# Optimization experiments

Measured on AMD Instinct MI355X. Metric: run time of the kernel, lower is better.

Reference implementation:

```python
import jax, jax.numpy as jnp
import numpy as np

# Model dims (see shape_source)
N, S, E, NMP, H, O = 20000, 16, 160000, 2, 4, 64
D_FEAT, E_DIM, PREP, NCLS, B = 64, 32, 128, 8, 4096
D1 = H * O  # 256, node/edge dim after layer 0


def setup_inputs() -> dict:
    key = jax.random.key(0)
    ks = jax.random.split(key, 24)
    g = lambda i, shape, fan: jax.random.normal(ks[i], shape, jnp.float32) * (fan ** -0.5)
    return {
        "feats": jax.random.normal(ks[0], (N, D_FEAT), jnp.float32),
        "edge_emb": jax.random.normal(ks[1], (NMP, E, E_DIM), jnp.float32),
        "W_prep0": g(2, (D_FEAT, PREP), D_FEAT),
        "W_prep1": g(3, (D_FEAT, PREP), D_FEAT),
        "edge_prep_w": g(4, (NMP, E_DIM, PREP), E_DIM),
        "edge_wq_l0": g(5, (NMP, H, PREP, O), PREP),
        "edge_wk_l0": g(6, (NMP, H, PREP, O), PREP),
        "edge_wq_l1": g(7, (NMP, H, D1, O), D1),
        "edge_wk_l1": g(8, (NMP, H, D1, O), D1),
        "node_wq_l0": g(9, (NMP, H, PREP, O), PREP),
        "node_wk_l0": g(10, (NMP, H, PREP, O), PREP),
        "node_wq_l1": g(11, (NMP, H, D1, O), D1),
        "node_wk_l1": g(12, (NMP, H, D1, O), D1),
        "Wg": g(13, (2 * D1, PREP), 2 * D1),
        "vg": g(14, (PREP,), PREP),
        "W_fc": g(15, (2 * D1, NCLS), 2 * D1),
        "b_fc": jnp.zeros((NCLS,), jnp.float32),
        "node2edge_idx": jax.random.randint(ks[20], (NMP, N, S), 0, E),
        "edge_node_adj": jax.random.randint(ks[21], (NMP, E, 2), 0, N),
        "train_ids": jax.random.randint(ks[22], (B,), 0, N),
    }


def _attn_agg(x_q, x_neigh, wq, wk):
    """Multi-head attention aggregator.
    x_q [M,d], x_neigh [M,s,d2], wq [H,d,O], wk [H,d2,O] -> [M, H*O]."""
    q = jnp.einsum('md,hdo->mho', x_q, wq)
    k = jnp.einsum('msd,hdo->msho', x_neigh, wk)
    logits = jnp.einsum('mho,msho->mhs', q, k) / np.float32(np.sqrt(O))
    a = jax.nn.softmax(logits, axis=-1)
    agg = jnp.einsum('mhs,msho->mho', a, k)
    out = jax.nn.elu(q + agg)
    return out.reshape(out.shape[0], H * O)


def reference(feats, edge_emb, W_prep0, W_prep1, edge_prep_w,
              edge_wq_l0, edge_wk_l0, edge_wq_l1, edge_wk_l1,
              node_wq_l0, node_wk_l0, node_wq_l1, node_wk_l1,
              Wg, vg, W_fc, b_fc,
              node2edge_idx, edge_node_adj, train_ids):
    e_wq, e_wk = [edge_wq_l0, edge_wq_l1], [edge_wk_l0, edge_wk_l1]
    n_wq, n_wk = [node_wq_l0, node_wq_l1], [node_wk_l0, node_wk_l1]
    outs = []
    for mp in range(NMP):  # small fixed count of message-passing branches
        dummy = feats @ W_prep0          # prep layer 0  [N,PREP]
        all_feats = feats @ W_prep1      # prep layer 1  [N,PREP]
        all_edges = edge_emb[mp] @ edge_prep_w[mp]  # [E,PREP]
        skip = []
        for l in range(2):  # depth
            # edge update: gather endpoint node feats [E,2,d], attend, concat heads
            neigh_nodes = all_feats[edge_node_adj[mp]]
            next_edges = _attn_agg(all_edges, neigh_nodes, e_wq[l][mp], e_wk[l][mp])
            # node update: gather incident edge feats [N,S,d] from OLD all_edges
            src = dummy if l == 0 else all_feats
            neigh_edges = all_edges[node2edge_idx[mp]]
            next_feats = _attn_agg(src, neigh_edges, n_wq[l][mp], n_wk[l][mp])
            skip.append(next_feats)
            all_feats, all_edges = next_feats, next_edges
        outs.append(jnp.concatenate(skip, axis=-1)[train_ids])  # [B, 2*D1]
    x = jnp.stack(outs, 0)  # [NMP, B, 512]
    # gated metapath aggregation (mp_agg): softmax over mp axis
    gate = jax.nn.softmax(jnp.einsum('mbe,e->mb', jnp.tanh(jnp.einsum('mbd,de->mbe', x, Wg)), vg), axis=0)
    pooled = jnp.einsum('mb,mbd->bd', gate, x)
    logits = pooled @ W_fc + b_fc  # [B, NCLS]
    return logits, gate
```

## Files before the change

### kernel.cpp

```cpp
#include <hip/hip_runtime.h>
#include <hip/hip_bf16.h>
#include <math.h>

#define N_NODES 20000
#define S_NE    16
#define E_EDGES 160000
#define NMP     2
#define H_HEADS 4
#define O_DIM   64
#define D_FEAT  64
#define E_DIMC  32
#define PREP    128
#define NCLS    8
#define B_TR    4096
#define D1      256
#define NSLOT   (B_TR * S_NE)

#define LDA0    132
#define LDA1    260
#define NPAD    264

typedef __hip_bfloat16 bf16;
typedef unsigned short u16;
typedef __attribute__((ext_vector_type(8))) short s8v;
// ... 115 lines not shown
        if (combo == 0) { qeh[dst] = hh; qel[dst] = ll; }
        else            { k0h[dst] = hh; k0l[dst] = ll; }
    } else if (combo == 2) {
        wkn[(size_t)mp * 64 * D1 + (size_t)r * D1 + n] = acc;
    } else {
        wq0[(size_t)mp * 64 * D1 + (size_t)r * D1 + n] = acc;
    }
}
__global__ void k_precomb2(const void* epw, const void* ewq, const void* nwk0,
                           const void* Wp1, const void* ewk,
                           const void* Wp0, const void* nwq0,
                           float* wkn, float* wq0,
                           u16* qeh, u16* qel, u16* k0h, u16* k0l,
                           const int* flag) {
    if (*flag == 1) precomb2_body<float>(epw, ewq, nwk0, Wp1, ewk, Wp0, nwq0, wkn, wq0, qeh, qel, k0h, k0l);
    else            precomb2_body<bf16 >(epw, ewq, nwk0, Wp1, ewk, Wp0, nwq0, wkn, wq0, qeh, qel, k0h, k0l);
}

template <typename T>
__device__ void embsplit_body(const void* emb, u16* eh, u16* el) {
    size_t idx = (size_t)blockIdx.x * 256 + threadIdx.x;
    if (idx >= (size_t)NMP * E_EDGES * E_DIMC) return;
    float v = ldv<T>(emb, idx);
    u16 hh, ll; splitbf(v, hh, ll);
    eh[idx] = hh; el[idx] = ll;
}
__global__ void k_embsplit(const void* emb, u16* eh, u16* el, const int* flag) {
    if (*flag == 1) embsplit_body<float>(emb, eh, el);
    else            embsplit_body<bf16 >(emb, eh, el);
}

template <typename T>
__device__ void wt1_body(const void* wk1, const void* wq1,
                         u16* kth, u16* ktl, u16* qth, u16* qtl) {
    int idx = blockIdx.x * 256 + threadIdx.x;
    int k = idx & 255, n = (idx >> 8) & 255;
    int wsel = (idx >> 16) & 1, mp = idx >> 17;
    size_t src = (size_t)mp * (H_HEADS * D1 * O_DIM) + (size_t)(n >> 6) * (D1 * O_DIM)
               + (size_t)k * O_DIM + (n & 63);
    float v = ldv<T>(wsel ? wq1 : wk1, src);
    u16 h, l; splitbf(v, h, l);
    size_t dst = (size_t)mp * 65536 + (size_t)n * 256 + k;
    if (wsel) { qth[dst] = h; qtl[dst] = l; }
    else      { kth[dst] = h; ktl[dst] = l; }
}
__global__ void k_wt1(const void* wk1, const void* wq1,
                      u16* kth, u16* ktl, u16* qth, u16* qtl, const int* flag) {
    if (*flag == 1) wt1_body<float>(wk1, wq1, kth, ktl, qth, qtl);
    else            wt1_body<bf16 >(wk1, wq1, kth, ktl, qth, qtl);
}

template <typename T>
__device__ void wgt_body(const void* Wg, u16* gh, u16* gl) {
    int idx = blockIdx.x * 256 + threadIdx.x;
    int n = idx >> 9, k = idx & 511;
    float v = ldv<T>(Wg, (size_t)k * PREP + n);
    u16 h, l; splitbf(v, h, l);
    gh[(size_t)n * 512 + k] = h;
    gl[(size_t)n * 512 + k] = l;
}
__global__ void k_wgt(const void* Wg, u16* gh, u16* gl, const int* flag) {
    if (*flag == 1) wgt_body<float>(Wg, gh, gl);
    else            wgt_body<bf16 >(Wg, gh, gl);
}

template <typename TA, typename TB>
__device__ void gemm_body(const void* A, size_t aOff, const int* Aidx, int strideA,
                          const void* B, int sH, int sD,
                          float* C, int ldC, int M, int K) {
    int bm = blockIdx.x * 64;
    int h  = blockIdx.y;
    int t  = threadIdx.x;
    int tx = t & 15, ty = t >> 4;

    __shared__ float As[32][68];
    __shared__ float Bs[32][68];

    float acc[4][4] = {{0.f}};
    int arow = t >> 3, kq = (t & 7) * 4;
    int brow = t >> 4, nq = (t & 15) * 4;

    for (int k0 = 0; k0 < K; k0 += 32) {
        #pragma unroll
        for (int c = 0; c < 2; ++c) {
            int rm = arow + 32 * c;
            int gr = bm + rm;
            gr = (gr < M) ? gr : 0;
            size_t row = Aidx ? (size_t)Aidx[gr] : (size_t)gr;
            float4 a = ld4<TA>(A, aOff + row * strideA + k0 + kq);
            As[kq + 0][rm] = a.x; As[kq + 1][rm] = a.y;
            As[kq + 2][rm] = a.z; As[kq + 3][rm] = a.w;
        }
        #pragma unroll
        for (int c = 0; c < 2; ++c) {
            int rk = brow + 16 * c;
            float4 b = ld4<TB>(B, (size_t)h * sH + (size_t)(k0 + rk) * sD + nq);
            *(float4*)&Bs[rk][nq] = b;
        }
        __syncthreads();
        #pragma unroll
        for (int kk = 0; kk < 32; ++kk) {
            float4 av = *(const float4*)&As[kk][ty * 4];
            float4 bv = *(const float4*)&Bs[kk][tx * 4];
            float am[4] = {av.x, av.y, av.z, av.w};
            #pragma unroll
            for (int i = 0; i < 4; ++i) {
                acc[i][0] += am[i] * bv.x; acc[i][1] += am[i] * bv.y;
                acc[i][2] += am[i] * bv.z; acc[i][3] += am[i] * bv.w;
            }
        }
        __syncthreads();
    }
    #pragma unroll
    for (int i = 0; i < 4; ++i) {
        int m = bm + ty * 4 + i;
        if (m < M) {
            float4 st; st.x = acc[i][0]; st.y = acc[i][1];
            st.z = acc[i][2]; st.w = acc[i][3];
            *(float4*)&C[(size_t)m * ldC + h * 64 + tx * 4] = st;
        }
    }
}
__global__ __launch_bounds__(256) void k_gemm_rf(
        const void* A, size_t aOff, const int* Aidx, int strideA,
        const float* B, int sH, int sD, float* C, int ldC, int M, int K,
        const int* flag) {
    if (*flag == 1) gemm_body<float, float>(A, aOff, Aidx, strideA, B, sH, sD, C, ldC, M, K);
    else            gemm_body<bf16,  float>(A, aOff, Aidx, strideA, B, sH, sD, C, ldC, M, K);
}

template <int K, bool G>
__device__ __forceinline__ void mfma_core(
        const u16* __restrict__ Ah, const u16* __restrict__ Al,
        const int* __restrict__ rows,
        const u16* __restrict__ Bh, const u16* __restrict__ Bl,
        int rbase, int bn, int lane, f4v acc[4][4]) {
    int fr = lane & 15;
    int kq = (lane >> 4) * 8;
    #pragma unroll
    for (int i = 0; i < 4; ++i)
        #pragma unroll
        for (int j = 0; j < 4; ++j) acc[i][j] = f4v{0.f, 0.f, 0.f, 0.f};
    #pragma unroll 2
    for (int k0 = 0; k0 < K; k0 += 32) {
        s8v ah[4], al[4], bh[4], bl[4];
        #pragma unroll
        for (int i = 0; i < 4; ++i) {
            size_t arow;
            if constexpr (G) arow = (size_t)rows[rbase + i * 16 + fr];
            else             arow = (size_t)(rbase + i * 16 + fr);
            size_t ao = arow * K + k0 + kq;
            ah[i] = *(const s8v*)(Ah + ao);
            al[i] = *(const s8v*)(Al + ao);
            size_t bo = (size_t)(bn + i * 16 + fr) * K + k0 + kq;
            bh[i] = *(const s8v*)(Bh + bo);
            bl[i] = *(const s8v*)(Bl + bo);
        }
        #pragma unroll
        for (int i = 0; i < 4; ++i)
            #pragma unroll
            for (int j = 0; j < 4; ++j) {
                acc[i][j] = __builtin_amdgcn_mfma_f32_16x16x32_bf16(al[i], bh[j], acc[i][j], 0, 0, 0);
                acc[i][j] = __builtin_amdgcn_mfma_f32_16x16x32_bf16(ah[i], bl[j], acc[i][j], 0, 0, 0);
                acc[i][j] = __builtin_amdgcn_mfma_f32_16x16x32_bf16(ah[i], bh[j], acc[i][j], 0, 0, 0);
            }
    }
}

template <int K>
__global__ __launch_bounds__(256) void k_mfma(
        const u16* __restrict__ Ah, const u16* __restrict__ Al,
        const u16* __restrict__ Bh, const u16* __restrict__ Bl,
        float* __restrict__ C, int ldC) {
    int w = threadIdx.x >> 6, lane = threadIdx.x & 63;
    int bm = blockIdx.x * 128 + (w & 1) * 64;
    int bn = blockIdx.y * 128 + (w >> 1) * 64;
    f4v acc[4][4];
    mfma_core<K, false>(Ah, Al, nullptr, Bh, Bl, bm, bn, lane, acc);
    int cn = lane & 15, cr = (lane >> 4) * 4;
    #pragma unroll
    for (int i = 0; i < 4; ++i) {
        int m0 = bm + i * 16 + cr;
        #pragma unroll
        for (int j = 0; j < 4; ++j) {
            int n = bn + j * 16 + cn;
            #pragma unroll
            for (int r = 0; r < 4; ++r)
                C[(size_t)(m0 + r) * ldC + n] = acc[i][j][r];
        }
    }
}

template <int K, bool G>
__global__ __launch_bounds__(256) void k_mfma_nattn(
        const u16* __restrict__ Ah, const u16* __restrict__ Al,
        const int* __restrict__ rows,
        const u16* __restrict__ Bh, const u16* __restrict__ Bl,
        const float* __restrict__ q,
        u16* __restrict__ o0h, u16* __restrict__ o0l,
        float* __restrict__ xrow, int xoff,
        u16* __restrict__ xh, u16* __restrict__ xl) {
    int w = threadIdx.x >> 6, lane = threadIdx.x & 63;
    int rbase = blockIdx.x * 128 + (w & 1) * 64;
    int bn = blockIdx.y * 128 + (w >> 1) * 64;
    f4v acc[4][4];
    mfma_core<K, G>(Ah, Al, rows, Bh, Bl, rbase, bn, lane, acc);

    int cn = lane & 15, grp = lane >> 4;
    #pragma unroll
    for (int i = 0; i < 4; ++i) {
        int b = (rbase >> 4) + i;
        float qv[4];
        #pragma unroll
        for (int j = 0; j < 4; ++j)
            qv[j] = q[(size_t)b * D1 + bn + j * 16 + cn];
        float lg[4];
        #pragma unroll
        for (int r = 0; r < 4; ++r) {
            float p = 0.f;
            #pragma unroll
            for (int j = 0; j < 4; ++j) p += acc[i][j][r] * qv[j];
            lg[r] = grp16_sum(p) * 0.125f;
        }
        float mx = fmaxf(fmaxf(lg[0], lg[1]), fmaxf(lg[2], lg[3]));
        mx = fmaxf(mx, __shfl_xor(mx, 16, 64));
        mx = fmaxf(mx, __shfl_xor(mx, 32, 64));
        float e[4], s = 0.f;
        #pragma unroll
        for (int r = 0; r < 4; ++r) { e[r] = expf(lg[r] - mx); s += e[r]; }
        s += __shfl_xor(s, 16, 64);
        s += __shfl_xor(s, 32, 64);
        float inv = 1.f / s;
        #pragma unroll
        for (int j = 0; j < 4; ++j) {
            float ag = e[0] * acc[i][j][0] + e[1] * acc[i][j][1]
                     + e[2] * acc[i][j][2] + e[3] * acc[i][j][3];
            ag += __shfl_xor(ag, 16, 64);
            ag += __shfl_xor(ag, 32, 64);
            float v = eluf(qv[j] + ag * inv);
            if (grp == 0) {
                int col = bn + j * 16 + cn;
                xrow[(size_t)b * (2 * D1) + xoff + col] = v;
                u16 hh, ll; splitbf(v, hh, ll);
                xh[(size_t)b * (2 * D1) + xoff + col] = hh;
                xl[(size_t)b * (2 * D1) + xoff + col] = ll;
                if (o0h) {
                    o0h[(size_t)b * D1 + col] = hh;
                    o0l[(size_t)b * D1 + col] = ll;
                }
            }
        }
    }
}

__global__ __launch_bounds__(512, 4) void k_mega(
        const u16* __restrict__ Ah, const u16* __restrict__ Al,
        const int* __restrict__ rows,
        const u16* __restrict__ qBh, const u16* __restrict__ qBl,
        const float* __restrict__ Kn,
        const int* __restrict__ adjA, const int* __restrict__ adjB,
        const u16* __restrict__ kBh, const u16* __restrict__ kBl,
        const float* __restrict__ q,
        float* __restrict__ xrow,
        u16* __restrict__ xh, u16* __restrict__ xl) {
    __shared__ u16 sh_[64][NPAD];
    __shared__ u16 sl_[64][NPAD];
    int w = threadIdx.x >> 6, lane = threadIdx.x & 63;
    int wr = w & 1, wc = w >> 1;
    int blk = blockIdx.x * 64;
    int rbase = blk + wr * 32;
    int bn = wc * 64;
    int fr = lane & 15, kq = (lane >> 4) * 8;
    int cn = lane & 15, cr = (lane >> 4) * 4;

    int raA[2][4], raB[2][4];
    #pragma unroll
    for (int i = 0; i < 2; ++i)
        #pragma unroll
        for (int r = 0; r < 4; ++r) {
            int slot = rbase + i * 16 + cr + r;
            raA[i][r] = adjA[slot] * D1;
            raB[i][r] = adjB[slot] * D1;
        }

    f4v acc[2][4];
    #pragma unroll
    for (int i = 0; i < 2; ++i)
        #pragma unroll
        for (int j = 0; j < 4; ++j) acc[i][j] = f4v{0.f, 0.f, 0.f, 0.f};
    {
        s8v ah[2], al[2], bh[4], bl[4];
        #pragma unroll
        for (int i = 0; i < 2; ++i) {
            size_t ao = (size_t)rows[rbase + i * 16 + fr] * E_DIMC + kq;
            ah[i] = *(const s8v*)(Ah + ao);
            al[i] = *(const s8v*)(Al + ao);
        }
        #pragma unroll
        for (int j = 0; j < 4; ++j) {
            size_t bo = (size_t)(bn + j * 16 + fr) * E_DIMC + kq;
            bh[j] = *(const s8v*)(qBh + bo);
            bl[j] = *(const s8v*)(qBl + bo);
        }
        #pragma unroll
        for (int i = 0; i < 2; ++i)
            #pragma unroll
            for (int j = 0; j < 4; ++j) {
                acc[i][j] = __builtin_amdgcn_mfma_f32_16x16x32_bf16(al[i], bh[j], acc[i][j], 0, 0, 0);
                acc[i][j] = __builtin_amdgcn_mfma_f32_16x16x32_bf16(ah[i], bl[j], acc[i][j], 0, 0, 0);
                acc[i][j] = __builtin_amdgcn_mfma_f32_16x16x32_bf16(ah[i], bh[j], acc[i][j], 0, 0, 0);
            }
    }

    #pragma unroll
    for (int i = 0; i < 2; ++i) {
        #pragma unroll
        for (int r = 0; r < 4; ++r) {
            int lrow = wr * 32 + i * 16 + cr + r;
            size_t ra = (size_t)raA[i][r];
            size_t rb = (size_t)raB[i][r];
            float kA[4], kB[4];
            float pA = 0.f, pB = 0.f;
            #pragma unroll
            for (int j = 0; j < 4; ++j) {
                int col = bn + j * 16 + cn;
                kA[j] = Kn[ra + col];
                kB[j] = Kn[rb + col];
                pA += acc[i][j][r] * kA[j];
                pB += acc[i][j][r] * kB[j];
            }
            float lA = grp16_sum(pA) * 0.125f;
            float lB = grp16_sum(pB) * 0.125f;
            float m = fmaxf(lA, lB);
            float eA = expf(lA - m), eB = expf(lB - m);
            float inv = 1.f / (eA + eB);
            #pragma unroll
            for (int j = 0; j < 4; ++j) {
                int col = bn + j * 16 + cn;
                float v = eluf(acc[i][j][r] + (eA * kA[j] + eB * kB[j]) * inv);
                u16 hh, ll; splitbf(v, hh, ll);
                sh_[lrow][col] = hh;
                sl_[lrow][col] = ll;
            }
        }
    }
    __syncthreads();

    #pragma unroll
    for (int i = 0; i < 2; ++i)
        #pragma unroll
        for (int j = 0; j < 4; ++j) acc[i][j] = f4v{0.f, 0.f, 0.f, 0.f};
    #pragma unroll 2
    for (int k0 = 0; k0 < 256; k0 += 32) {
        s8v ah[2], al[2], bh[4], bl[4];
        #pragma unroll
        for (int i = 0; i < 2; ++i) {
            int lr = wr * 32 + i * 16 + fr;
            ah[i] = *(const s8v*)&sh_[lr][k0 + kq];
            al[i] = *(const s8v*)&sl_[lr][k0 + kq];
        }
        #pragma unroll
        for (int j = 0; j < 4; ++j) {
            size_t bo = (size_t)(bn + j * 16 + fr) * 256 + k0 + kq;
            bh[j] = *(const s8v*)(kBh + bo);
            bl[j] = *(const s8v*)(kBl + bo);
        }
        #pragma unroll
        for (int i = 0; i < 2; ++i)
            #pragma unroll
            for (int j = 0; j < 4; ++j) {
                acc[i][j] = __builtin_amdgcn_mfma_f32_16x16x32_bf16(al[i], bh[j], acc[i][j], 0, 0, 0);
                acc[i][j] = __builtin_amdgcn_mfma_f32_16x16x32_bf16(ah[i], bl[j], acc[i][j], 0, 0, 0);
                acc[i][j] = __builtin_amdgcn_mfma_f32_16x16x32_bf16(ah[i], bh[j], acc[i][j], 0, 0, 0);
            }
    }

    int grp = lane >> 4;
    #pragma unroll
    for (int i = 0; i < 2; ++i) {
        int b = (rbase >> 4) + i;
        float qv[4];
        #pragma unroll
        for (int j = 0; j < 4; ++j)
            qv[j] = q[(size_t)b * D1 + bn + j * 16 + cn];
        float lg[4];
        #pragma unroll
        for (int r = 0; r < 4; ++r) {
            float p = 0.f;
            #pragma unroll
            for (int j = 0; j < 4; ++j) p += acc[i][j][r] * qv[j];
            lg[r] = grp16_sum(p) * 0.125f;
        }
        float mx = fmaxf(fmaxf(lg[0], lg[1]), fmaxf(lg[2], lg[3]));
        mx = fmaxf(mx, __shfl_xor(mx, 16, 64));
        mx = fmaxf(mx, __shfl_xor(mx, 32, 64));
        float e[4], s = 0.f;
        #pragma unroll
        for (int r = 0; r < 4; ++r) { e[r] = expf(lg[r] - mx); s += e[r]; }
        s += __shfl_xor(s, 16, 64);
        s += __shfl_xor(s, 32, 64);
        float inv = 1.f / s;
        #pragma unroll
        for (int j = 0; j < 4; ++j) {
            float ag = e[0] * acc[i][j][0] + e[1] * acc[i][j][1]
                     + e[2] * acc[i][j][2] + e[3] * acc[i][j][3];
            ag += __shfl_xor(ag, 16, 64);
            ag += __shfl_xor(ag, 32, 64);
            float v = eluf(qv[j] + ag * inv);
            if (grp == 0) {
                int col = bn + j * 16 + cn;
                xrow[(size_t)b * (2 * D1) + D1 + col] = v;
                u16 hh, ll; splitbf(v, hh, ll);
                xh[(size_t)b * (2 * D1) + D1 + col] = hh;
                xl[(size_t)b * (2 * D1) + D1 + col] = ll;
            }
        }
    }
}

__global__ void k_slot_setup(const int* __restrict__ n2e_mp,
                             const int* __restrict__ adj_mp,
                             const int* __restrict__ tid,
                             int* __restrict__ eid,
                             int* __restrict__ adjA,
                             int* __restrict__ adjB) {
    int i = blockIdx.x * blockDim.x + threadIdx.x;
    if (i >= NSLOT) return;
    int b = i >> 4, s = i & 15;
    int e = n2e_mp[(size_t)tid[b] * S_NE + s];
    eid[i] = e;
    adjA[i] = adj_mp[(size_t)e * 2 + 0];
    adjB[i] = adj_mp[(size_t)e * 2 + 1];
}

template <typename T>
__device__ void gate_fin_body(const float* gmat, const void* vg, float* gate_pre) {
    int row = blockIdx.x;
    int t = threadIdx.x;
    float v = tanhf(gmat[(size_t)row * PREP + t]) * ldv<T>(vg, t);
    __shared__ float red[128];
    red[t] = v;
    __syncthreads();
    for (int s = 64; s > 0; s >>= 1) { if (t < s) red[t] += red[t + s]; __syncthreads(); }
    if (t == 0) gate_pre[row] = red[0];
}
__global__ void k_gate_fin(const float* gmat, const void* vg, float* gate_pre,
                           const int* flag) {
    if (*flag == 1) gate_fin_body<float>(gmat, vg, gate_pre);
    else            gate_fin_body<bf16 >(gmat, vg, gate_pre);
}

template <typename T>
__device__ void gate_dir_body(const float* xcat, const void* Wg, const void* vg,
                              float* gate_pre) {
    int mb = blockIdx.x;
    int t = threadIdx.x;
    __shared__ float xr[2 * D1];
    for (int idx = t; idx < 2 * D1; idx += 128) xr[idx] = xcat[(size_t)mb * (2 * D1) + idx];
    __syncthreads();
    float acc = 0.f;
    for (int d = 0; d < 2 * D1; ++d) acc += xr[d] * ldv<T>(Wg, (size_t)d * PREP + t);
    float gp = tanhf(acc) * ldv<T>(vg, t);
    __shared__ float red[128];
    red[t] = gp;
    __syncthreads();
// ... 295 lines not shown
    const void* e_wk0       = d_in[6];
    const void* n_wq0       = d_in[9];
    const void* n_wk0       = d_in[10];
    const void* n_wq1       = d_in[11];
    const void* n_wk1       = d_in[12];
    const void* Wg          = d_in[13];
    const void* vg          = d_in[14];
    const void* Wfc         = d_in[15];
    const void* bfc         = d_in[16];
    const int*  n2e         = (const int*)d_in[17];
    const int*  adj         = (const int*)d_in[18];
    const int*  tid         = (const int*)d_in[19];

    float* ws   = (float*)d_ws;
    int*   flag = (int*)ws;
    float* base = ws + 4;
    size_t avail = (ws_size >= 16) ? (ws_size - 16) / 4 : 0;

    k_detect<<<1, 64, 0, stream>>>((const unsigned*)feats, flag);

    size_t off = 0;
    auto alloc = [&](size_t n) { size_t o = off; off += (n + 3) & ~(size_t)3; return o; };
    size_t o_xcat = alloc((size_t)NMP * B_TR * 2 * D1);
    size_t o_gmat = alloc((size_t)NMP * B_TR * PREP);
    size_t o_gpre = alloc(NMP * B_TR);
    size_t o_wkn  = alloc(NMP * 64 * D1);
    size_t o_wq0  = alloc(NMP * 64 * D1);
    size_t o_qeh  = alloc(NMP * 256 * 32 / 2);
    size_t o_qel  = alloc(NMP * 256 * 32 / 2);
    size_t o_k0h  = alloc(NMP * 256 * 32 / 2);
    size_t o_k0l  = alloc(NMP * 256 * 32 / 2);
    size_t o_ebh  = alloc((size_t)NMP * E_EDGES * E_DIMC / 2);
    size_t o_ebl  = alloc((size_t)NMP * E_EDGES * E_DIMC / 2);
    size_t o_Kn   = alloc((size_t)N_NODES * D1);
    size_t o_q0   = alloc((size_t)B_TR * D1);
    size_t o_Q1   = alloc((size_t)B_TR * D1);
    size_t o_eid  = alloc(NSLOT);
    size_t o_adjA = alloc(NSLOT);
    size_t o_adjB = alloc(NSLOT);
    size_t o_o0h  = alloc((size_t)B_TR * D1 / 2);
    size_t o_o0l  = alloc((size_t)B_TR * D1 / 2);
    size_t o_xh   = alloc((size_t)NMP * B_TR * D1);
    size_t o_xl   = alloc((size_t)NMP * B_TR * D1);
    size_t o_wk1h = alloc((size_t)NMP * 32768);
    size_t o_wk1l = alloc((size_t)NMP * 32768);
    size_t o_wq1h = alloc((size_t)NMP * 32768);
    size_t o_wq1l = alloc((size_t)NMP * 32768);
    size_t o_wgh  = alloc(32768);
    size_t o_wgl  = alloc(32768);
    size_t fixed = off;

    int CH = (fixed <= avail) ? B_TR : 0;

    if (CH > 0) {
        float* xcat = base + o_xcat;
        float* gmat = base + o_gmat;
        float* gpre = base + o_gpre;
        float* wkn  = base + o_wkn;
        float* wq0  = base + o_wq0;
        u16*   qeh  = (u16*)(base + o_qeh);
        u16*   qel  = (u16*)(base + o_qel);
        u16*   k0h  = (u16*)(base + o_k0h);
        u16*   k0l  = (u16*)(base + o_k0l);
        u16*   ebh  = (u16*)(base + o_ebh);
        u16*   ebl  = (u16*)(base + o_ebl);
        float* Kn   = base + o_Kn;
        float* q0   = base + o_q0;
        float* Q1   = base + o_Q1;
        int*   eid  = (int*)(base + o_eid);
        int*   adjA = (int*)(base + o_adjA);
        int*   adjB = (int*)(base + o_adjB);
        u16*   o0h  = (u16*)(base + o_o0h);
        u16*   o0l  = (u16*)(base + o_o0l);
        u16*   xh   = (u16*)(base + o_xh);
        u16*   xl   = (u16*)(base + o_xl);
        u16*   wk1h = (u16*)(base + o_wk1h);
        u16*   wk1l = (u16*)(base + o_wk1l);
        u16*   wq1h = (u16*)(base + o_wq1h);
        u16*   wq1l = (u16*)(base + o_wq1l);
        u16*   wgh  = (u16*)(base + o_wgh);
        u16*   wgl  = (u16*)(base + o_wgl);
        int NC = B_TR / CH;

        k_precomb2<<<384, 256, 0, stream>>>(edge_prep_w, e_wq0, n_wk0, W_prep1,
                                            e_wk0, W_prep0, n_wq0,
                                            wkn, wq0, qeh, qel, k0h, k0l, flag);
        k_embsplit<<<(NMP * E_EDGES * E_DIMC + 255) / 256, 256, 0, stream>>>(
            edge_emb, ebh, ebl, flag);
        k_wt1<<<1024, 256, 0, stream>>>(n_wk1, n_wq1, wk1h, wk1l, wq1h, wq1l, flag);
        k_wgt<<<256, 256, 0, stream>>>(Wg, wgh, wgl, flag);

        for (int mp = 0; mp < NMP; ++mp) {
            k_slot_setup<<<(NSLOT + 255) / 256, 256, 0, stream>>>(
                n2e + (size_t)mp * N_NODES * S_NE,
                adj + (size_t)mp * E_EDGES * 2,
                tid, eid, adjA, adjB);

            k_gemm_rf<<<dim3((N_NODES + 63) / 64, 4), 256, 0, stream>>>(
                feats, 0, nullptr, D_FEAT, wkn + (size_t)mp * 64 * D1,
                64, D1, Kn, D1, N_NODES, D_FEAT, flag);
            k_gemm_rf<<<dim3(B_TR / 64, 4), 256, 0, stream>>>(
                feats, 0, tid, D_FEAT, wq0 + (size_t)mp * 64 * D1,
                64, D1, q0, D1, B_TR, D_FEAT, flag);

            const u16* ebh_mp = ebh + (size_t)mp * E_EDGES * E_DIMC;
            const u16* ebl_mp = ebl + (size_t)mp * E_EDGES * E_DIMC;

            for (int c = 0; c < NC; ++c) {
                int c0 = c * CH;
                int MS = CH * S_NE;
                k_mfma_nattn<32, true><<<dim3(MS / 128, 2), 256, 0, stream>>>(
                    ebh_mp, ebl_mp, eid + (size_t)c0 * S_NE,
                    k0h + (size_t)mp * 8192, k0l + (size_t)mp * 8192,
                    q0 + (size_t)c0 * D1, o0h, o0l,
                    xcat + ((size_t)mp * B_TR + c0) * 2 * D1, 0,
                    xh + ((size_t)mp * B_TR + c0) * 2 * D1,
                    xl + ((size_t)mp * B_TR + c0) * 2 * D1);
                k_mfma<256><<<dim3(CH / 128, 2), 256, 0, stream>>>(
                    o0h, o0l, wq1h + (size_t)mp * 65536, wq1l + (size_t)mp * 65536,
                    Q1, D1);
                k_mega<<<MS / 64, 512, 0, stream>>>(
                    ebh_mp, ebl_mp, eid + (size_t)c0 * S_NE,
                    qeh + (size_t)mp * 8192, qel + (size_t)mp * 8192,
                    Kn, adjA + (size_t)c0 * S_NE, adjB + (size_t)c0 * S_NE,
                    wk1h + (size_t)mp * 65536, wk1l + (size_t)mp * 65536,
                    Q1,
                    xcat + ((size_t)mp * B_TR + c0) * 2 * D1,
                    xh + ((size_t)mp * B_TR + c0) * 2 * D1,
                    xl + ((size_t)mp * B_TR + c0) * 2 * D1);
            }
        }
        k_mfma<512><<<dim3(NMP * B_TR / 128, 1), 256, 0, stream>>>(
            xh, xl, wgh, wgl, gmat, PREP);
        k_gate_fin<<<NMP * B_TR, 128, 0, stream>>>(gmat, vg, gpre, flag);
        k_final<<<B_TR, 64, 0, stream>>>(xcat, gpre, Wfc, bfc, d_out, flag);
    } else {
        size_t f_off = 0;
        auto falloc = [&](size_t n) { size_t o = f_off; f_off += (n + 3) & ~(size_t)3; return o; };
        float* af0  = base + falloc((size_t)N_NODES * PREP);
        float* xcat = base + falloc((size_t)NMP * B_TR * 2 * D1);
        float* gpre = base + falloc(NMP * B_TR);

        k_prep_nodes<float><<<(N_NODES * 32 + 255) / 256, 256, 0, stream>>>(
            feats, W_prep1, af0, flag);
        k_prep_nodes<bf16><<<(N_NODES * 32 + 255) / 256, 256, 0, stream>>>(
            feats, W_prep1, af0, flag);

        for (int mp = 0; mp < NMP; ++mp) {
            #define FUSED_ARGS(esz)                                                   \
                feats,                                                                \
                (const char*)edge_emb + (esz) * (size_t)mp * E_EDGES * E_DIMC,        \
                W_prep0,                                                              \
                (const char*)edge_prep_w + (esz) * (size_t)mp * E_DIMC * PREP,        \
                (const char*)e_wq0 + (esz) * (size_t)mp * H_HEADS * PREP * O_DIM,     \
                (const char*)e_wk0 + (esz) * (size_t)mp * H_HEADS * PREP * O_DIM,     \
                (const char*)n_wq0 + (esz) * (size_t)mp * H_HEADS * PREP * O_DIM,     \
                (const char*)n_wk0 + (esz) * (size_t)mp * H_HEADS * PREP * O_DIM,     \
                (const char*)n_wq1 + (esz) * (size_t)mp * H_HEADS * D1 * O_DIM,       \
                (const char*)n_wk1 + (esz) * (size_t)mp * H_HEADS * D1 * O_DIM,       \
                n2e + (size_t)mp * N_NODES * S_NE,                                    \
                adj + (size_t)mp * E_EDGES * 2,                                       \
                tid, af0, xcat + (size_t)mp * B_TR * 2 * D1, flag
            k_fused<float><<<B_TR, 256, 0, stream>>>(FUSED_ARGS(4));
            k_fused<bf16><<<B_TR, 256, 0, stream>>>(FUSED_ARGS(2));
// ... 7 lines not shown
```

Baseline: 528.9 us.

## Fuse layer-0 node attention and Q1 projection into mega kernel

Merges the layer-0 node attention kernel, the Q1 GEMM and the layer-1 mega kernel into one kernel per metapath. The layer-0 output now stays in shared memory, and Q1 is computed in-block by an fp32 dot product against a transposed fp32 copy of wq1. This removes the chunk loop, two launches per chunk and the intermediate global buffers. In exchange, the Q1 projection moves from split-bf16 MFMA to scalar FMAs, with each block re-reading the full 256x256 weight column set, and shared memory use grows.

Result: no change. 532.7 us (+0.7%).

```diff
diff --git a/kernel.cpp b/kernel.cpp
--- a/kernel.cpp
+++ b/kernel.cpp
@@ -171,7 +171,7 @@
 
 template <typename T>
 __device__ void wt1_body(const void* wk1, const void* wq1,
-                         u16* kth, u16* ktl, u16* qth, u16* qtl) {
+                         u16* kth, u16* ktl, u16* qth, u16* qtl, float* wq1f) {
     int idx = blockIdx.x * 256 + threadIdx.x;
     int k = idx & 255, n = (idx >> 8) & 255;
     int wsel = (idx >> 16) & 1, mp = idx >> 17;
@@ -180,13 +180,18 @@
     float v = ldv<T>(wsel ? wq1 : wk1, src);
     u16 h, l; splitbf(v, h, l);
     size_t dst = (size_t)mp * 65536 + (size_t)n * 256 + k;
-    if (wsel) { qth[dst] = h; qtl[dst] = l; }
-    else      { kth[dst] = h; ktl[dst] = l; }
+    if (wsel) {
+        qth[dst] = h; qtl[dst] = l;
+        wq1f[(size_t)mp * 65536 + (size_t)k * 256 + n] = v;
+    } else {
+        kth[dst] = h; ktl[dst] = l;
+    }
 }
 __global__ void k_wt1(const void* wk1, const void* wq1,
-                      u16* kth, u16* ktl, u16* qth, u16* qtl, const int* flag) {
-    if (*flag == 1) wt1_body<float>(wk1, wq1, kth, ktl, qth, qtl);
-    else            wt1_body<bf16 >(wk1, wq1, kth, ktl, qth, qtl);
+                      u16* kth, u16* ktl, u16* qth, u16* qtl, float* wq1f,
+                      const int* flag) {
+    if (*flag == 1) wt1_body<float>(wk1, wq1, kth, ktl, qth, qtl, wq1f);
+    else            wt1_body<bf16 >(wk1, wq1, kth, ktl, qth, qtl, wq1f);
 }
 
 template <typename T>
@@ -330,29 +335,81 @@
     }
 }
 
-template <int K, bool G>
-__global__ __launch_bounds__(256) void k_mfma_nattn(
+__global__ __launch_bounds__(512, 4) void k_mega2(
         const u16* __restrict__ Ah, const u16* __restrict__ Al,
         const int* __restrict__ rows,
-        const u16* __restrict__ Bh, const u16* __restrict__ Bl,
-        const float* __restrict__ q,
-        u16* __restrict__ o0h, u16* __restrict__ o0l,
-        float* __restrict__ xrow, int xoff,
+        const u16* __restrict__ k0Bh, const u16* __restrict__ k0Bl,
+        const u16* __restrict__ qBh,  const u16* __restrict__ qBl,
+        const float* __restrict__ q0,
+        const float* __restrict__ Kn,
+        const int* __restrict__ adjA, const int* __restrict__ adjB,
+        const u16* __restrict__ kBh, const u16* __restrict__ kBl,
+        const float* __restrict__ wq1f,
+        float* __restrict__ xrow,
         u16* __restrict__ xh, u16* __restrict__ xl) {
+    __shared__ u16 sh_[64][NPAD];
+    __shared__ u16 sl_[64][NPAD];
+    __shared__ float s_o0[4][D1];
+    __shared__ float s_q1[4][D1];
     int w = threadIdx.x >> 6, lane = threadIdx.x & 63;
-    int rbase = blockIdx.x * 128 + (w & 1) * 64;
-    int bn = blockIdx.y * 128 + (w >> 1) * 64;
-    f4v acc[4][4];
-    mfma_core<K, G>(Ah, Al, rows, Bh, Bl, rbase, bn, lane, acc);
-
-    int cn = lane & 15, grp = lane >> 4;
-    #pragma unroll
-    for (int i = 0; i < 4; ++i) {
-        int b = (rbase >> 4) + i;
+    int wr = w & 1, wc = w >> 1;
+    int blk = blockIdx.x * 64;
+    int rbase = blk + wr * 32;
+    int bn = wc * 64;
+    int fr = lane & 15, kq = (lane >> 4) * 8;
+    int cn = lane & 15, cr = (lane >> 4) * 4;
+    int grp = lane >> 4;
+
+    int raA[2][4], raB[2][4];
+    #pragma unroll
+    for (int i = 0; i < 2; ++i)
+        #pragma unroll
+        for (int r = 0; r < 4; ++r) {
+            int slot = rbase + i * 16 + cr + r;
+            raA[i][r] = adjA[slot] * D1;
+            raB[i][r] = adjB[slot] * D1;
+        }
+
+    s8v ebh2[2], ebl2[2];
+    #pragma unroll
+    for (int i = 0; i < 2; ++i) {
+        size_t ao = (size_t)rows[rbase + i * 16 + fr] * E_DIMC + kq;
+        ebh2[i] = *(const s8v*)(Ah + ao);
+        ebl2[i] = *(const s8v*)(Al + ao);
+    }
+
+    f4v acc[2][4];
+
+    #pragma unroll
+    for (int i = 0; i < 2; ++i)
+        #pragma unroll
+        for (int j = 0; j < 4; ++j) acc[i][j] = f4v{0.f, 0.f, 0.f, 0.f};
+    {
+        s8v bh[4], bl[4];
+        #pragma unroll
+        for (int j = 0; j < 4; ++j) {
+            size_t bo = (size_t)(bn + j * 16 + fr) * E_DIMC + kq;
+            bh[j] = *(const s8v*)(k0Bh + bo);
+            bl[j] = *(const s8v*)(k0Bl + bo);
+        }
+        #pragma unroll
+        for (int i = 0; i < 2; ++i)
+            #pragma unroll
+            for (int j = 0; j < 4; ++j) {
+                acc[i][j] = __builtin_amdgcn_mfma_f32_16x16x32_bf16(ebl2[i], bh[j], acc[i][j], 0, 0, 0);
+                acc[i][j] = __builtin_amdgcn_mfma_f32_16x16x32_bf16(ebh2[i], bl[j], acc[i][j], 0, 0, 0);
+                acc[i][j] = __builtin_amdgcn_mfma_f32_16x16x32_bf16(ebh2[i], bh[j], acc[i][j], 0, 0, 0);
+            }
+    }
+
+    #pragma unroll
+    for (int i = 0; i < 2; ++i) {
+        int b  = (rbase >> 4) + i;
+        int lb = wr * 2 + i;
         float qv[4];
         #pragma unroll
         for (int j = 0; j < 4; ++j)
-            qv[j] = q[(size_t)b * D1 + bn + j * 16 + cn];
+            qv[j] = q0[(size_t)b * D1 + bn + j * 16 + cn];
         float lg[4];
         #pragma unroll
         for (int r = 0; r < 4; ++r) {
@@ -379,62 +436,22 @@
             float v = eluf(qv[j] + ag * inv);
             if (grp == 0) {
                 int col = bn + j * 16 + cn;
-                xrow[(size_t)b * (2 * D1) + xoff + col] = v;
+                xrow[(size_t)b * (2 * D1) + col] = v;
                 u16 hh, ll; splitbf(v, hh, ll);
-                xh[(size_t)b * (2 * D1) + xoff + col] = hh;
-                xl[(size_t)b * (2 * D1) + xoff + col] = ll;
-                if (o0h) {
-                    o0h[(size_t)b * D1 + col] = hh;
-                    o0l[(size_t)b * D1 + col] = ll;
-                }
-            }
-        }
-    }
-}
-
-__global__ __launch_bounds__(512, 4) void k_mega(
-        const u16* __restrict__ Ah, const u16* __restrict__ Al,
-        const int* __restrict__ rows,
-        const u16* __restrict__ qBh, const u16* __restrict__ qBl,
-        const float* __restrict__ Kn,
-        const int* __restrict__ adjA, const int* __restrict__ adjB,
-        const u16* __restrict__ kBh, const u16* __restrict__ kBl,
-        const float* __restrict__ q,
-        float* __restrict__ xrow,
-        u16* __restrict__ xh, u16* __restrict__ xl) {
-    __shared__ u16 sh_[64][NPAD];
-    __shared__ u16 sl_[64][NPAD];
-    int w = threadIdx.x >> 6, lane = threadIdx.x & 63;
-    int wr = w & 1, wc = w >> 1;
-    int blk = blockIdx.x * 64;
-    int rbase = blk + wr * 32;
-    int bn = wc * 64;
-    int fr = lane & 15, kq = (lane >> 4) * 8;
-    int cn = lane & 15, cr = (lane >> 4) * 4;
-
-    int raA[2][4], raB[2][4];
-    #pragma unroll
-    for (int i = 0; i < 2; ++i)
-        #pragma unroll
-        for (int r = 0; r < 4; ++r) {
-            int slot = rbase + i * 16 + cr + r;
-            raA[i][r] = adjA[slot] * D1;
-            raB[i][r] = adjB[slot] * D1;
-        }
-
-    f4v acc[2][4];
+                xh[(size_t)b * (2 * D1) + col] = hh;
+                xl[(size_t)b * (2 * D1) + col] = ll;
+                s_o0[lb][col] = v;
+            }
+        }
+    }
+    __syncthreads();
+
     #pragma unroll
     for (int i = 0; i < 2; ++i)
         #pragma unroll
         for (int j = 0; j < 4; ++j) acc[i][j] = f4v{0.f, 0.f, 0.f, 0.f};
     {
-        s8v ah[2], al[2], bh[4], bl[4];
-        #pragma unroll
-        for (int i = 0; i < 2; ++i) {
-            size_t ao = (size_t)rows[rbase + i * 16 + fr] * E_DIMC + kq;
-            ah[i] = *(const s8v*)(Ah + ao);
-            al[i] = *(const s8v*)(Al + ao);
-        }
+        s8v bh[4], bl[4];
         #pragma unroll
         for (int j = 0; j < 4; ++j) {
             size_t bo = (size_t)(bn + j * 16 + fr) * E_DIMC + kq;
@@ -445,10 +462,24 @@
         for (int i = 0; i < 2; ++i)
             #pragma unroll
             for (int j = 0; j < 4; ++j) {
-                acc[i][j] = __builtin_amdgcn_mfma_f32_16x16x32_bf16(al[i], bh[j], acc[i][j], 0, 0, 0);
-                acc[i][j] = __builtin_amdgcn_mfma_f32_16x16x32_bf16(ah[i], bl[j], acc[i][j], 0, 0, 0);
-                acc[i][j] = __builtin_amdgcn_mfma_f32_16x16x32_bf16(ah[i], bh[j], acc[i][j], 0, 0, 0);
-            }
+                acc[i][j] = __builtin_amdgcn_mfma_f32_16x16x32_bf16(ebl2[i], bh[j], acc[i][j], 0, 0, 0);
+                acc[i][j] = __builtin_amdgcn_mfma_f32_16x16x32_bf16(ebh2[i], bl[j], acc[i][j], 0, 0, 0);
+                acc[i][j] = __builtin_amdgcn_mfma_f32_16x16x32_bf16(ebh2[i], bh[j], acc[i][j], 0, 0, 0);
+            }
+    }
+
+    {
+        int lb0 = wr * 2, lb1 = lb0 + 1;
+        float q1a = 0.f, q1b = 0.f;
+        const float* wcol = wq1f + bn + lane;
+        #pragma unroll 4
+        for (int k = 0; k < D1; ++k) {
+            float wv = wcol[(size_t)k * D1];
+            q1a += s_o0[lb0][k] * wv;
+            q1b += s_o0[lb1][k] * wv;
+        }
+        s_q1[lb0][bn + lane] = q1a;
+        s_q1[lb1][bn + lane] = q1b;
     }
 
     #pragma unroll
@@ -514,14 +545,14 @@
             }
     }
 
-    int grp = lane >> 4;
     #pragma unroll
     for (int i = 0; i < 2; ++i) {
-        int b = (rbase >> 4) + i;
+        int b  = (rbase >> 4) + i;
+        int lb = wr * 2 + i;
         float qv[4];
         #pragma unroll
         for (int j = 0; j < 4; ++j)
-            qv[j] = q[(size_t)b * D1 + bn + j * 16 + cn];
+            qv[j] = s_q1[lb][bn + j * 16 + cn];
         float lg[4];
         #pragma unroll
         for (int r = 0; r < 4; ++r) {
@@ -933,18 +964,16 @@
     size_t o_ebl  = alloc((size_t)NMP * E_EDGES * E_DIMC / 2);
     size_t o_Kn   = alloc((size_t)N_NODES * D1);
     size_t o_q0   = alloc((size_t)B_TR * D1);
-    size_t o_Q1   = alloc((size_t)B_TR * D1);
     size_t o_eid  = alloc(NSLOT);
     size_t o_adjA = alloc(NSLOT);
     size_t o_adjB = alloc(NSLOT);
-    size_t o_o0h  = alloc((size_t)B_TR * D1 / 2);
-    size_t o_o0l  = alloc((size_t)B_TR * D1 / 2);
     size_t o_xh   = alloc((size_t)NMP * B_TR * D1);
     size_t o_xl   = alloc((size_t)NMP * B_TR * D1);
     size_t o_wk1h = alloc((size_t)NMP * 32768);
     size_t o_wk1l = alloc((size_t)NMP * 32768);
     size_t o_wq1h = alloc((size_t)NMP * 32768);
     size_t o_wq1l = alloc((size_t)NMP * 32768);
+    size_t o_wq1f = alloc((size_t)NMP * 65536);
     size_t o_wgh  = alloc(32768);
     size_t o_wgl  = alloc(32768);
     size_t fixed = off;
@@ -965,28 +994,26 @@
         u16*   ebl  = (u16*)(base + o_ebl);
         float* Kn   = base + o_Kn;
         float* q0   = base + o_q0;
-        float* Q1   = base + o_Q1;
         int*   eid  = (int*)(base + o_eid);
         int*   adjA = (int*)(base + o_adjA);
         int*   adjB = (int*)(base + o_adjB);
-        u16*   o0h  = (u16*)(base + o_o0h);
-        u16*   o0l  = (u16*)(base + o_o0l);
         u16*   xh   = (u16*)(base + o_xh);
         u16*   xl   = (u16*)(base + o_xl);
         u16*   wk1h = (u16*)(base + o_wk1h);
         u16*   wk1l = (u16*)(base + o_wk1l);
         u16*   wq1h = (u16*)(base + o_wq1h);
         u16*   wq1l = (u16*)(base + o_wq1l);
+        float* wq1f = base + o_wq1f;
         u16*   wgh  = (u16*)(base + o_wgh);
         u16*   wgl  = (u16*)(base + o_wgl);
-        int NC = B_TR / CH;
 
         k_precomb2<<<384, 256, 0, stream>>>(edge_prep_w, e_wq0, n_wk0, W_prep1,
                                             e_wk0, W_prep0, n_wq0,
                                             wkn, wq0, qeh, qel, k0h, k0l, flag);
         k_embsplit<<<(NMP * E_EDGES * E_DIMC + 255) / 256, 256, 0, stream>>>(
             edge_emb, ebh, ebl, flag);
-        k_wt1<<<1024, 256, 0, stream>>>(n_wk1, n_wq1, wk1h, wk1l, wq1h, wq1l, flag);
+        k_wt1<<<1024, 256, 0, stream>>>(n_wk1, n_wq1, wk1h, wk1l, wq1h, wq1l,
+                                        wq1f, flag);
         k_wgt<<<256, 256, 0, stream>>>(Wg, wgh, wgl, flag);
 
         for (int mp = 0; mp < NMP; ++mp) {
@@ -1002,32 +1029,18 @@
                 feats, 0, tid, D_FEAT, wq0 + (size_t)mp * 64 * D1,
                 64, D1, q0, D1, B_TR, D_FEAT, flag);
 
-            const u16* ebh_mp = ebh + (size_t)mp * E_EDGES * E_DIMC;
-            const u16* ebl_mp = ebl + (size_t)mp * E_EDGES * E_DIMC;
-
-            for (int c = 0; c < NC; ++c) {
-                int c0 = c * CH;
-                int MS = CH * S_NE;
-                k_mfma_nattn<32, true><<<dim3(MS / 128, 2), 256, 0, stream>>>(
-                    ebh_mp, ebl_mp, eid + (size_t)c0 * S_NE,
-                    k0h + (size_t)mp * 8192, k0l + (size_t)mp * 8192,
-                    q0 + (size_t)c0 * D1, o0h, o0l,
-                    xcat + ((size_t)mp * B_TR + c0) * 2 * D1, 0,
-                    xh + ((size_t)mp * B_TR + c0) * 2 * D1,
-                    xl + ((size_t)mp * B_TR + c0) * 2 * D1);
-                k_mfma<256><<<dim3(CH / 128, 2), 256, 0, stream>>>(
-                    o0h, o0l, wq1h + (size_t)mp * 65536, wq1l + (size_t)mp * 65536,
-                    Q1, D1);
-                k_mega<<<MS / 64, 512, 0, stream>>>(
-                    ebh_mp, ebl_mp, eid + (size_t)c0 * S_NE,
-                    qeh + (size_t)mp * 8192, qel + (size_t)mp * 8192,
-                    Kn, adjA + (size_t)c0 * S_NE, adjB + (size_t)c0 * S_NE,
-                    wk1h + (size_t)mp * 65536, wk1l + (size_t)mp * 65536,
-                    Q1,
-                    xcat + ((size_t)mp * B_TR + c0) * 2 * D1,
-                    xh + ((size_t)mp * B_TR + c0) * 2 * D1,
-                    xl + ((size_t)mp * B_TR + c0) * 2 * D1);
-            }
+            k_mega2<<<NSLOT / 64, 512, 0, stream>>>(
+                ebh + (size_t)mp * E_EDGES * E_DIMC,
+                ebl + (size_t)mp * E_EDGES * E_DIMC,
+                eid,
+                k0h + (size_t)mp * 8192, k0l + (size_t)mp * 8192,
+                qeh + (size_t)mp * 8192, qel + (size_t)mp * 8192,
+                q0, Kn, adjA, adjB,
+                wk1h + (size_t)mp * 65536, wk1l + (size_t)mp * 65536,
+                wq1f + (size_t)mp * 65536,
+                xcat + (size_t)mp * B_TR * 2 * D1,
+                xh + (size_t)mp * B_TR * 2 * D1,
+                xl + (size_t)mp * B_TR * 2 * D1);
         }
         k_mfma<512><<<dim3(NMP * B_TR / 128, 1), 256, 0, stream>>>(
             xh, xl, wgh, wgl, gmat, PREP);
```

## Batch both metapaths and all chunks into single grid-z launches

Applied to the files above, without the earlier changes.

Replaces the host loop over metapaths and batch chunks with single launches that use blockIdx.z to select the metapath, and processes the whole batch at once. Intermediate buffers (Kn, q0, Q1, slot indices, o0) are enlarged to hold both metapaths. This cuts kernel launch count and gives each kernel a larger grid for better GPU occupancy, at the cost of more scratch memory and a larger working set.

Result: faster. 492.5 us, median of 3 (-6.9%).

```diff
diff --git a/kernel.cpp b/kernel.cpp
--- a/kernel.cpp
+++ b/kernel.cpp
@@ -205,7 +205,7 @@
 
 template <typename TA, typename TB>
 __device__ void gemm_body(const void* A, size_t aOff, const int* Aidx, int strideA,
-                          const void* B, int sH, int sD,
+                          const float* B, int sH, int sD,
                           float* C, int ldC, int M, int K) {
     int bm = blockIdx.x * 64;
     int h  = blockIdx.y;
@@ -233,7 +233,7 @@
         #pragma unroll
         for (int c = 0; c < 2; ++c) {
             int rk = brow + 16 * c;
-            float4 b = ld4<TB>(B, (size_t)h * sH + (size_t)(k0 + rk) * sD + nq);
+            float4 b = ld4<float>(B, (size_t)h * sH + (size_t)(k0 + rk) * sD + nq);
             *(float4*)&Bs[rk][nq] = b;
         }
         __syncthreads();
@@ -262,10 +262,13 @@
 }
 __global__ __launch_bounds__(256) void k_gemm_rf(
         const void* A, size_t aOff, const int* Aidx, int strideA,
-        const float* B, int sH, int sD, float* C, int ldC, int M, int K,
+        const float* B, size_t bStride, int sH, int sD,
+        float* C, size_t cStride, int ldC, int M, int K,
         const int* flag) {
-    if (*flag == 1) gemm_body<float, float>(A, aOff, Aidx, strideA, B, sH, sD, C, ldC, M, K);
-    else            gemm_body<bf16,  float>(A, aOff, Aidx, strideA, B, sH, sD, C, ldC, M, K);
+    const float* Bz = B + (size_t)blockIdx.z * bStride;
+    float* Cz = C + (size_t)blockIdx.z * cStride;
+    if (*flag == 1) gemm_body<float, float>(A, aOff, Aidx, strideA, Bz, sH, sD, Cz, ldC, M, K);
+    else            gemm_body<bf16,  float>(A, aOff, Aidx, strideA, Bz, sH, sD, Cz, ldC, M, K);
 }
 
 template <int K, bool G>
@@ -330,20 +333,60 @@
     }
 }
 
-template <int K, bool G>
-__global__ __launch_bounds__(256) void k_mfma_nattn(
-        const u16* __restrict__ Ah, const u16* __restrict__ Al,
-        const int* __restrict__ rows,
-        const u16* __restrict__ Bh, const u16* __restrict__ Bl,
-        const float* __restrict__ q,
-        u16* __restrict__ o0h, u16* __restrict__ o0l,
-        float* __restrict__ xrow, int xoff,
-        u16* __restrict__ xh, u16* __restrict__ xl) {
+__global__ __launch_bounds__(256) void k_q1(
+        const u16* __restrict__ o0h, const u16* __restrict__ o0l,
+        const u16* __restrict__ qth, const u16* __restrict__ qtl,
+        float* __restrict__ Q1) {
+    int mp = blockIdx.z;
+    const u16* Ah = o0h + (size_t)mp * B_TR * D1;
+    const u16* Al = o0l + (size_t)mp * B_TR * D1;
+    const u16* Bh = qth + (size_t)mp * 65536;
+    const u16* Bl = qtl + (size_t)mp * 65536;
+    float* C = Q1 + (size_t)mp * B_TR * D1;
+    int w = threadIdx.x >> 6, lane = threadIdx.x & 63;
+    int bm = blockIdx.x * 128 + (w & 1) * 64;
+    int bn = blockIdx.y * 128 + (w >> 1) * 64;
+    f4v acc[4][4];
+    mfma_core<256, false>(Ah, Al, nullptr, Bh, Bl, bm, bn, lane, acc);
+    int cn = lane & 15, cr = (lane >> 4) * 4;
+    #pragma unroll
+    for (int i = 0; i < 4; ++i) {
+        int m0 = bm + i * 16 + cr;
+        #pragma unroll
+        for (int j = 0; j < 4; ++j) {
+            int n = bn + j * 16 + cn;
+            #pragma unroll
+            for (int r = 0; r < 4; ++r)
+                C[(size_t)(m0 + r) * D1 + n] = acc[i][j][r];
+        }
+    }
+}
+
+__global__ __launch_bounds__(256) void k_nattn0(
+        const u16* __restrict__ ebh, const u16* __restrict__ ebl,
+        const int* __restrict__ eid,
+        const u16* __restrict__ k0h, const u16* __restrict__ k0l,
+        const float* __restrict__ q0b,
+        u16* __restrict__ o0hb, u16* __restrict__ o0lb,
+        float* __restrict__ xcat, u16* __restrict__ xhb, u16* __restrict__ xlb) {
+    int mp = blockIdx.z;
+    const u16* Ah = ebh + (size_t)mp * E_EDGES * E_DIMC;
+    const u16* Al = ebl + (size_t)mp * E_EDGES * E_DIMC;
+    const int* rows = eid + (size_t)mp * NSLOT;
+    const u16* Bh = k0h + (size_t)mp * 8192;
+    const u16* Bl = k0l + (size_t)mp * 8192;
+    const float* q = q0b + (size_t)mp * B_TR * D1;
+    u16* o0h = o0hb + (size_t)mp * B_TR * D1;
+    u16* o0l = o0lb + (size_t)mp * B_TR * D1;
+    float* xrow = xcat + (size_t)mp * B_TR * 2 * D1;
+    u16* xh = xhb + (size_t)mp * B_TR * 2 * D1;
+    u16* xl = xlb + (size_t)mp * B_TR * 2 * D1;
+
     int w = threadIdx.x >> 6, lane = threadIdx.x & 63;
     int rbase = blockIdx.x * 128 + (w & 1) * 64;
     int bn = blockIdx.y * 128 + (w >> 1) * 64;
     f4v acc[4][4];
-    mfma_core<K, G>(Ah, Al, rows, Bh, Bl, rbase, bn, lane, acc);
+    mfma_core<32, true>(Ah, Al, rows, Bh, Bl, rbase, bn, lane, acc);
 
     int cn = lane & 15, grp = lane >> 4;
     #pragma unroll
@@ -379,29 +422,42 @@
             float v = eluf(qv[j] + ag * inv);
             if (grp == 0) {
                 int col = bn + j * 16 + cn;
-                xrow[(size_t)b * (2 * D1) + xoff + col] = v;
+                xrow[(size_t)b * (2 * D1) + col] = v;
                 u16 hh, ll; splitbf(v, hh, ll);
-                xh[(size_t)b * (2 * D1) + xoff + col] = hh;
-                xl[(size_t)b * (2 * D1) + xoff + col] = ll;
-                if (o0h) {
-                    o0h[(size_t)b * D1 + col] = hh;
-                    o0l[(size_t)b * D1 + col] = ll;
-                }
+                xh[(size_t)b * (2 * D1) + col] = hh;
+                xl[(size_t)b * (2 * D1) + col] = ll;
+                o0h[(size_t)b * D1 + col] = hh;
+                o0l[(size_t)b * D1 + col] = ll;
             }
         }
     }
 }
 
 __global__ __launch_bounds__(512, 4) void k_mega(
-        const u16* __restrict__ Ah, const u16* __restrict__ Al,
-        const int* __restrict__ rows,
-        const u16* __restrict__ qBh, const u16* __restrict__ qBl,
-        const float* __restrict__ Kn,
-        const int* __restrict__ adjA, const int* __restrict__ adjB,
-        const u16* __restrict__ kBh, const u16* __restrict__ kBl,
-        const float* __restrict__ q,
-        float* __restrict__ xrow,
-        u16* __restrict__ xh, u16* __restrict__ xl) {
+        const u16* __restrict__ ebh, const u16* __restrict__ ebl,
+        const int* __restrict__ eid,
+        const u16* __restrict__ qeh, const u16* __restrict__ qel,
+        const float* __restrict__ Knb,
+        const int* __restrict__ adjAb, const int* __restrict__ adjBb,
+        const u16* __restrict__ kth, const u16* __restrict__ ktl,
+        const float* __restrict__ Q1b,
+        float* __restrict__ xcat, u16* __restrict__ xhb, u16* __restrict__ xlb) {
+    int mp = blockIdx.z;
+    const u16* Ah = ebh + (size_t)mp * E_EDGES * E_DIMC;
+    const u16* Al = ebl + (size_t)mp * E_EDGES * E_DIMC;
+    const int* rows = eid + (size_t)mp * NSLOT;
+    const u16* qBh = qeh + (size_t)mp * 8192;
+    const u16* qBl = qel + (size_t)mp * 8192;
+    const float* Kn = Knb + (size_t)mp * N_NODES * D1;
+    const int* adjA = adjAb + (size_t)mp * NSLOT;
+    const int* adjB = adjBb + (size_t)mp * NSLOT;
+    const u16* kBh = kth + (size_t)mp * 65536;
+    const u16* kBl = ktl + (size_t)mp * 65536;
+    const float* q = Q1b + (size_t)mp * B_TR * D1;
+    float* xrow = xcat + (size_t)mp * B_TR * 2 * D1;
+    u16* xh = xhb + (size_t)mp * B_TR * 2 * D1;
+    u16* xl = xlb + (size_t)mp * B_TR * 2 * D1;
+
     __shared__ u16 sh_[64][NPAD];
     __shared__ u16 sl_[64][NPAD];
     int w = threadIdx.x >> 6, lane = threadIdx.x & 63;
@@ -557,19 +613,20 @@
     }
 }
 
-__global__ void k_slot_setup(const int* __restrict__ n2e_mp,
-                             const int* __restrict__ adj_mp,
-                             const int* __restrict__ tid,
-                             int* __restrict__ eid,
-                             int* __restrict__ adjA,
-                             int* __restrict__ adjB) {
+__global__ void k_slot_setup2(const int* __restrict__ n2e,
+                              const int* __restrict__ adj,
+                              const int* __restrict__ tid,
+                              int* __restrict__ eid,
+                              int* __restrict__ adjA,
+                              int* __restrict__ adjB) {
     int i = blockIdx.x * blockDim.x + threadIdx.x;
-    if (i >= NSLOT) return;
-    int b = i >> 4, s = i & 15;
-    int e = n2e_mp[(size_t)tid[b] * S_NE + s];
+    if (i >= NMP * NSLOT) return;
+    int mp = i / NSLOT, sl = i - mp * NSLOT;
+    int b = sl >> 4, s = sl & 15;
+    int e = n2e[(size_t)mp * N_NODES * S_NE + (size_t)tid[b] * S_NE + s];
     eid[i] = e;
-    adjA[i] = adj_mp[(size_t)e * 2 + 0];
-    adjB[i] = adj_mp[(size_t)e * 2 + 1];
+    adjA[i] = adj[(size_t)mp * E_EDGES * 2 + (size_t)e * 2 + 0];
+    adjB[i] = adj[(size_t)mp * E_EDGES * 2 + (size_t)e * 2 + 1];
 }
 
 template <typename T>
@@ -931,14 +988,14 @@
     size_t o_k0l  = alloc(NMP * 256 * 32 / 2);
     size_t o_ebh  = alloc((size_t)NMP * E_EDGES * E_DIMC / 2);
     size_t o_ebl  = alloc((size_t)NMP * E_EDGES * E_DIMC / 2);
-    size_t o_Kn   = alloc((size_t)N_NODES * D1);
-    size_t o_q0   = alloc((size_t)B_TR * D1);
-    size_t o_Q1   = alloc((size_t)B_TR * D1);
-    size_t o_eid  = alloc(NSLOT);
-    size_t o_adjA = alloc(NSLOT);
-    size_t o_adjB = alloc(NSLOT);
-    size_t o_o0h  = alloc((size_t)B_TR * D1 / 2);
-    size_t o_o0l  = alloc((size_t)B_TR * D1 / 2);
+    size_t o_Kn   = alloc((size_t)NMP * N_NODES * D1);
+    size_t o_q0   = alloc((size_t)NMP * B_TR * D1);
+    size_t o_Q1   = alloc((size_t)NMP * B_TR * D1);
+    size_t o_eid  = alloc((size_t)NMP * NSLOT);
+    size_t o_adjA = alloc((size_t)NMP * NSLOT);
+    size_t o_adjB = alloc((size_t)NMP * NSLOT);
+    size_t o_o0h  = alloc((size_t)NMP * B_TR * D1 / 2);
+    size_t o_o0l  = alloc((size_t)NMP * B_TR * D1 / 2);
     size_t o_xh   = alloc((size_t)NMP * B_TR * D1);
     size_t o_xl   = alloc((size_t)NMP * B_TR * D1);
     size_t o_wk1h = alloc((size_t)NMP * 32768);
@@ -979,7 +1036,6 @@
         u16*   wq1l = (u16*)(base + o_wq1l);
         u16*   wgh  = (u16*)(base + o_wgh);
         u16*   wgl  = (u16*)(base + o_wgl);
-        int NC = B_TR / CH;
 
         k_precomb2<<<384, 256, 0, stream>>>(edge_prep_w, e_wq0, n_wk0, W_prep1,
                                             e_wk0, W_prep0, n_wq0,
@@ -988,47 +1044,25 @@
             edge_emb, ebh, ebl, flag);
         k_wt1<<<1024, 256, 0, stream>>>(n_wk1, n_wq1, wk1h, wk1l, wq1h, wq1l, flag);
         k_wgt<<<256, 256, 0, stream>>>(Wg, wgh, wgl, flag);
-
-        for (int mp = 0; mp < NMP; ++mp) {
-            k_slot_setup<<<(NSLOT + 255) / 256, 256, 0, stream>>>(
-                n2e + (size_t)mp * N_NODES * S_NE,
-                adj + (size_t)mp * E_EDGES * 2,
-                tid, eid, adjA, adjB);
-
-            k_gemm_rf<<<dim3((N_NODES + 63) / 64, 4), 256, 0, stream>>>(
-                feats, 0, nullptr, D_FEAT, wkn + (size_t)mp * 64 * D1,
-                64, D1, Kn, D1, N_NODES, D_FEAT, flag);
-            k_gemm_rf<<<dim3(B_TR / 64, 4), 256, 0, stream>>>(
-                feats, 0, tid, D_FEAT, wq0 + (size_t)mp * 64 * D1,
-                64, D1, q0, D1, B_TR, D_FEAT, flag);
-
-            const u16* ebh_mp = ebh + (size_t)mp * E_EDGES * E_DIMC;
-            const u16* ebl_mp = ebl + (size_t)mp * E_EDGES * E_DIMC;
-
-            for (int c = 0; c < NC; ++c) {
-                int c0 = c * CH;
-                int MS = CH * S_NE;
-                k_mfma_nattn<32, true><<<dim3(MS / 128, 2), 256, 0, stream>>>(
-                    ebh_mp, ebl_mp, eid + (size_t)c0 * S_NE,
-                    k0h + (size_t)mp * 8192, k0l + (size_t)mp * 8192,
-                    q0 + (size_t)c0 * D1, o0h, o0l,
-                    xcat + ((size_t)mp * B_TR + c0) * 2 * D1, 0,
-                    xh + ((size_t)mp * B_TR + c0) * 2 * D1,
-                    xl + ((size_t)mp * B_TR + c0) * 2 * D1);
-                k_mfma<256><<<dim3(CH / 128, 2), 256, 0, stream>>>(
-                    o0h, o0l, wq1h + (size_t)mp * 65536, wq1l + (size_t)mp * 65536,
-                    Q1, D1);
-                k_mega<<<MS / 64, 512, 0, stream>>>(
-                    ebh_mp, ebl_mp, eid + (size_t)c0 * S_NE,
-                    qeh + (size_t)mp * 8192, qel + (size_t)mp * 8192,
-                    Kn, adjA + (size_t)c0 * S_NE, adjB + (size_t)c0 * S_NE,
-                    wk1h + (size_t)mp * 65536, wk1l + (size_t)mp * 65536,
-                    Q1,
-                    xcat + ((size_t)mp * B_TR + c0) * 2 * D1,
-                    xh + ((size_t)mp * B_TR + c0) * 2 * D1,
-                    xl + ((size_t)mp * B_TR + c0) * 2 * D1);
-            }
-        }
+        k_slot_setup2<<<(NMP * NSLOT + 255) / 256, 256, 0, stream>>>(
+            n2e, adj, tid, eid, adjA, adjB);
+
+        k_gemm_rf<<<dim3((N_NODES + 63) / 64, 4, NMP), 256, 0, stream>>>(
+            feats, 0, nullptr, D_FEAT,
+            wkn, (size_t)64 * D1, 64, D1,
+            Kn, (size_t)N_NODES * D1, D1, N_NODES, D_FEAT, flag);
+        k_gemm_rf<<<dim3(B_TR / 64, 4, NMP), 256, 0, stream>>>(
+            feats, 0, tid, D_FEAT,
+            wq0, (size_t)64 * D1, 64, D1,
+            q0, (size_t)B_TR * D1, D1, B_TR, D_FEAT, flag);
+        k_nattn0<<<dim3(NSLOT / 128, 2, NMP), 256, 0, stream>>>(
+            ebh, ebl, eid, k0h, k0l, q0, o0h, o0l, xcat, xh, xl);
+        k_q1<<<dim3(B_TR / 128, 2, NMP), 256, 0, stream>>>(
+            o0h, o0l, wq1h, wq1l, Q1);
+        k_mega<<<dim3(NSLOT / 64, 1, NMP), 512, 0, stream>>>(
+            ebh, ebl, eid, qeh, qel, Kn, adjA, adjB,
+            wk1h, wk1l, Q1, xcat, xh, xl);
+
         k_mfma<512><<<dim3(NMP * B_TR / 128, 1), 256, 0, stream>>>(
             xh, xl, wgh, wgl, gmat, PREP);
         k_gate_fin<<<NMP * B_TR, 128, 0, stream>>>(gmat, vg, gpre, flag);
```
